# Optimization experiments

Hardware: AMD Instinct MI355X
Metric: run time of the kernel (lower is better)

The kernel has to match this reference:

```python
import jax, jax.numpy as jnp
from jax import lax
import numpy as np


def _fps(xyz, M):
    # Farthest point sampling: sequential over M steps, vectorized over batch.
    B, N, _ = xyz.shape
    def body(carry, _):
        dists, far = carry                       # dists:[B,N], far:[B]
        c = xyz[jnp.arange(B), far]              # [B,3] current centroid
        d = jnp.sum((xyz - c[:, None, :]) ** 2, axis=-1)
        dists = jnp.minimum(dists, d)
        nxt = jnp.argmax(dists, axis=-1).astype(jnp.int32)
        return (dists, nxt), far
    init = (jnp.full((B, N), 1e10, xyz.dtype), jnp.zeros((B,), jnp.int32))
    _, inds = lax.scan(body, init, None, length=M)
    return inds.T                                # [B, M]


def _ball_query(xyz, new_xyz, radius, K):
    # For each centroid pick first K point indices within radius; pad with first hit.
    N = xyz.shape[1]
    d2 = jnp.sum((new_xyz[:, :, None, :] - xyz[:, None, :, :]) ** 2, axis=-1)  # [B,M,N]
    ids = jnp.where(d2 <= radius * radius, jnp.arange(N)[None, None, :], N)
    ids = jnp.sort(ids, axis=-1)[..., :K]        # [B,M,K]
    return jnp.where(ids == N, ids[..., :1], ids)


_gather = jax.vmap(lambda p, i: p[i])            # p:[N,C], i:[M,K] -> [M,K,C]


def _mlp(x, layers):
    # Shared per-point MLP (1x1 conv + ReLU chain); BN omitted as in source head.
    for w, b in layers:
        x = jax.nn.relu(jnp.einsum('bmkc,cd->bmkd', x, w) + b)
    return x


def _sa(xyz, points, M, radius, K, layers):
    # Set-abstraction: FPS -> ball query -> group (centered xyz ++ feats) -> MLP -> max over K.
    fi = _fps(xyz, M)                                        # [B,M]
    new_xyz = jnp.take_along_axis(xyz, fi[..., None], axis=1)  # [B,M,3]
    gi = _ball_query(xyz, new_xyz, radius, K)                # [B,M,K]
    g_xyz = _gather(xyz, gi) - new_xyz[:, :, None, :]        # [B,M,K,3]
    g = jnp.concatenate([g_xyz, _gather(points, gi)], axis=-1)
    return new_xyz, jnp.max(_mlp(g, layers), axis=2)         # [B,M,Cout]


def _forward(xyz, points,
             w1a, b1a, w1b, b1b, w1c, b1c,
             w2a, b2a, w2b, b2b, w2c, b2c,
             w3a, b3a, w3b, b3b, w3c, b3c,
             lin1_w, lin2_w, cls_w, cls_b):
    B = xyz.shape[0]
    x1, f1 = _sa(xyz, points, 512, 0.2, 32, [(w1a, b1a), (w1b, b1b), (w1c, b1c)])
    x2, f2 = _sa(x1, f1, 128, 0.4, 64, [(w2a, b2a), (w2b, b2b), (w2c, b2c)])
    # group_all: single group containing all 128 points, feats = [xyz ++ points] (259 ch)
    g = jnp.concatenate([x2, f2], axis=-1)[:, None]           # [B,1,128,259]
    f3 = jnp.max(_mlp(g, [(w3a, b3a), (w3b, b3b), (w3c, b3c)]), axis=2)  # [B,1,1024]
    net = f3.reshape(B, -1)
    net = jax.nn.relu(net @ lin1_w)   # linear1 (no bias) + ReLU; dropout=identity (eval)
    net = jax.nn.relu(net @ lin2_w)
    return net @ cls_w + cls_b


def setup_inputs() -> dict:
    key = jax.random.key(0)
    ks = iter(jax.random.split(key, 40))
    B, N, NC = 32, 1024, 40
    inp = {}
    inp['xyz'] = jax.random.uniform(next(ks), (B, N, 3), jnp.float32, -1.0, 1.0)
    inp['points'] = jax.random.normal(next(ks), (B, N, 3), jnp.float32)
    def lin(cin, cout):
        w = jax.random.normal(next(ks), (cin, cout), jnp.float32) / np.float32(np.sqrt(cin))
        return w, jnp.zeros((cout,), jnp.float32)
    dims = {'1': [(6, 64), (64, 64), (64, 128)],
            '2': [(131, 128), (128, 128), (128, 256)],
            '3': [(259, 256), (256, 512), (512, 1024)]}
    for s, layer_dims in dims.items():
        for tag, (ci, co) in zip('abc', layer_dims):
            w, b = lin(ci, co)
            inp['w%s%s' % (s, tag)] = w
            inp['b%s%s' % (s, tag)] = b
    inp['lin1_w'] = jax.random.normal(next(ks), (1024, 512), jnp.float32) / np.float32(32.0)
    inp['lin2_w'] = jax.random.normal(next(ks), (512, 256), jnp.float32) / np.float32(np.sqrt(512))
    inp['cls_w'] = jax.random.normal(next(ks), (256, NC), jnp.float32) / np.float32(16.0)
    inp['cls_b'] = jnp.zeros((NC,), jnp.float32)
    return inp


def reference(xyz, points,
              w1a, b1a, w1b, b1b, w1c, b1c,
              w2a, b2a, w2b, b2b, w2c, b2c,
              w3a, b3a, w3b, b3b, w3c, b3c,
              lin1_w, lin2_w, cls_w, cls_b):
    return _forward(xyz, points,
                    w1a, b1a, w1b, b1b, w1c, b1c,
                    w2a, b2a, w2b, b2b, w2c, b2c,
                    w3a, b3a, w3b, b3b, w3c, b3c,
                    lin1_w, lin2_w, cls_w, cls_b)
```

## Files before the change

kernel.cpp:

```cpp
#include <hip/hip_runtime.h>

#define DEVFN __device__ __forceinline__

static inline int ceil_div(int a, int b) { return (a + b - 1) / b; }

typedef __attribute__((ext_vector_type(8))) short         bf16x8;
typedef __attribute__((ext_vector_type(4))) float         f32x4;
typedef __attribute__((ext_vector_type(8))) unsigned short u16x8;

DEVFN unsigned short f2bf(float x) {
    unsigned u = __float_as_uint(x);
    unsigned r = ((u >> 16) & 1u) + 0x7fffu;
    return (unsigned short)((u + r) >> 16);
}
DEVFN float bf2f(unsigned short h) { return __uint_as_float(((unsigned)h) << 16); }

template<int CTRL>
DEVFN double dpp_max_step(double v)
{
    int lo = __double2loint(v), hi = __double2hiint(v);
    int tlo = __builtin_amdgcn_update_dpp(lo, lo, CTRL, 0xF, 0xF, false);
    int thi = __builtin_amdgcn_update_dpp(hi, hi, CTRL, 0xF, 0xF, false);
    return fmax(v, __hiloint2double(thi, tlo));
}

template<int N>
__global__ __launch_bounds__(64) void fps_kernel(const float* __restrict__ xyz, int M,
                                                 int* __restrict__ out_idx,
                                                 float* __restrict__ nxout)
{
    constexpr int PPL = N / 64;
    int b = blockIdx.x, lane = threadIdx.x;
    __shared__ float4 sp[N];
    const float* p = xyz + (size_t)b * N * 3;
    float px[PPL], py[PPL], pz[PPL], dd[PPL];
    unsigned lo[PPL];
    #pragma unroll
    for (int j = 0; j < PPL; ++j) {
        int idx = lane + 64 * j;
        px[j] = p[idx*3+0]; py[j] = p[idx*3+1]; pz[j] = p[idx*3+2];
        sp[idx] = make_float4(px[j], py[j], pz[j], 0.f);
        dd[j] = 1e10f;
        lo[j] = ~(unsigned)idx;
    }
    __syncthreads();
    int far = 0;
    for (int s = 0; s < M; ++s) {
        float4 c4 = sp[far];
        if (lane == 0) {
            out_idx[(size_t)b*M + s] = far;
            nxout[((size_t)b*M + s)*3 + 0] = c4.x;
            nxout[((size_t)b*M + s)*3 + 1] = c4.y;
            nxout[((size_t)b*M + s)*3 + 2] = c4.z;
        }
        double cand[PPL];
        #pragma unroll
        for (int j = 0; j < PPL; ++j) {
            float dx = __fsub_rn(px[j], c4.x);
            float dy = __fsub_rn(py[j], c4.y);
            float dz = __fsub_rn(pz[j], c4.z);
            float d  = __fadd_rn(__fadd_rn(__fmul_rn(dx,dx), __fmul_rn(dy,dy)),
                                 __fmul_rn(dz,dz));
            float nd = fminf(dd[j], d);
            dd[j] = nd;
            cand[j] = __hiloint2double(__float_as_int(nd), (int)lo[j]);
        }
        #pragma unroll
        for (int st = PPL/2; st > 0; st >>= 1)
            #pragma unroll
            for (int j = 0; j < PPL; ++j)
                if (j < st) cand[j] = fmax(cand[j], cand[j + st]);
        double v = cand[0];
        v = dpp_max_step<0xB1>(v);
        v = dpp_max_step<0x4E>(v);
        v = dpp_max_step<0x124>(v);
        v = dpp_max_step<0x128>(v);
        v = dpp_max_step<0x142>(v);
        v = dpp_max_step<0x143>(v);
        int wlo = __builtin_amdgcn_readlane(__double2loint(v), 63);
        far = (int)(~(unsigned)wlo);
    }
}

__global__ void ballquery_kernel(const float* __restrict__ xyz,
                                 const float* __restrict__ new_xyz,
                                 int* __restrict__ gi,
                                 int B, int N, int M, int K, float r2)
{
    int t = blockIdx.x * blockDim.x + threadIdx.x;
    if (t >= B * M) return;
    int b = t / M;
    const float* p = xyz + (size_t)b * N * 3;
    float cx = new_xyz[t*3+0], cy = new_xyz[t*3+1], cz = new_xyz[t*3+2];
    int* out = gi + (size_t)t * K;
    int cnt = 0, first = 0;
    bool havefirst = false;
    for (int i = 0; i < N; ++i) {
        float dx = __fsub_rn(p[i*3+0], cx);
        float dy = __fsub_rn(p[i*3+1], cy);
        float dz = __fsub_rn(p[i*3+2], cz);
        float d  = __fadd_rn(__fadd_rn(__fmul_rn(dx,dx), __fmul_rn(dy,dy)),
                             __fmul_rn(dz,dz));
        if (d <= r2) {
            if (!havefirst) { first = i; havefirst = true; }
            out[cnt++] = i;
            if (cnt == K) break;
        }
    }
    for (; cnt < K; ++cnt) out[cnt] = first;
}

DEVFN float f4_elem(const float4& v, int u) {
    return u == 0 ? v.x : u == 1 ? v.y : u == 2 ? v.z : v.w;
}

__global__ void wsplit_kernel(const float* __restrict__ w,
                              unsigned short* __restrict__ wh,
                              unsigned short* __restrict__ wl, int CI, int CO)
{
    int t = blockIdx.x * 256 + threadIdx.x;
    if (t >= CI * CO) return;
    int co = t / CI, ci = t % CI;
    float v = w[(size_t)ci * CO + co];
    unsigned short h = f2bf(v);
    wh[t] = h;
    wl[t] = f2bf(v - bf2f(h));
}

__global__ void asplit_kernel(const float* __restrict__ a,
                              unsigned short* __restrict__ ah,
                              unsigned short* __restrict__ al, int n)
{
    int t = blockIdx.x * 256 + threadIdx.x;
    if (t >= n) return;
    float v = a[t];
    unsigned short h = f2bf(v);
    ah[t] = h;
    al[t] = f2bf(v - bf2f(h));
}

template<int CF, int CO, int KPTS>
__global__ __launch_bounds__(256) void sa_l1_kernel(
    const float* __restrict__ xyz, const float* __restrict__ feats,
    const float* __restrict__ new_xyz, const int* __restrict__ gi,
    const float* __restrict__ w, const float* __restrict__ bias,
    unsigned short* __restrict__ oh, unsigned short* __restrict__ ol,
    int N, int M, int row0)
{
    constexpr int WCH = CO / 4;
    const int lane = threadIdx.x & 63;
    const int wv   = __builtin_amdgcn_readfirstlane(threadIdx.x >> 6);
    const int rl   = blockIdx.x * 64 + lane;
    const int row  = row0 + rl;
    const int cent = row / KPTS;
    const int b    = cent / M;
    const int idx  = gi[row];
    const float* pp  = xyz + ((size_t)b*N + idx)*3;
    const float* cc3 = new_xyz + (size_t)cent*3;
    float a0 = __fsub_rn(pp[0], cc3[0]);
    float a1 = __fsub_rn(pp[1], cc3[1]);
    float a2 = __fsub_rn(pp[2], cc3[2]);
    const float* frow = feats + ((size_t)b*N + idx)*CF;
    const float* wcol = w + wv*WCH;
    const float* bcol = bias + wv*WCH;
    float acc[WCH];
    #pragma unroll
    for (int j = 0; j < WCH; ++j) acc[j] = bcol[j];
    #pragma unroll
    for (int j = 0; j < WCH; ++j) acc[j] += a0 * wcol[0*CO + j];
    #pragma unroll
    for (int j = 0; j < WCH; ++j) acc[j] += a1 * wcol[1*CO + j];
    #pragma unroll
    for (int j = 0; j < WCH; ++j) acc[j] += a2 * wcol[2*CO + j];
    constexpr int CF4 = CF & ~3;
    #pragma unroll 2
    for (int cc = 0; cc < CF4; cc += 4) {
        float4 a4 = *(const float4*)(frow + cc);
        #pragma unroll
        for (int u = 0; u < 4; ++u) {
            float a = f4_elem(a4, u);
            #pragma unroll
            for (int j = 0; j < WCH; ++j)
                acc[j] += a * wcol[(size_t)(3 + cc + u)*CO + j];
        }
    }
    #pragma unroll
    for (int f = CF4; f < CF; ++f) {
        float a = frow[f];
        #pragma unroll
        for (int j = 0; j < WCH; ++j)
            acc[j] += a * wcol[(size_t)(3 + f)*CO + j];
    }
    #pragma unroll
    for (int j8 = 0; j8 < WCH; j8 += 8) {
        u16x8 hv, lv;
        #pragma unroll
        for (int u = 0; u < 8; ++u) {
            float v = fmaxf(acc[j8+u], 0.f);
            unsigned short h = f2bf(v);
            hv[u] = (unsigned short)h;
            lv[u] = f2bf(v - bf2f(h));
        }
        size_t o = (size_t)rl*CO + wv*WCH + j8;
        *(u16x8*)(&oh[o]) = hv;
        *(u16x8*)(&ol[o]) = lv;
    }
}

template<int CI, int CO, int NTILE, int MROW, int KPTS, int OUTMODE>
__global__ __launch_bounds__(256) void mfma_layer_kernel(
    const unsigned short* __restrict__ ah, const unsigned short* __restrict__ al,
    const unsigned short* __restrict__ wh, const unsigned short* __restrict__ wl,
    const float* __restrict__ bias,
    unsigned short* __restrict__ oh, unsigned short* __restrict__ ol,
    float* __restrict__ ofp, int rowbase)
{
    constexpr int KT = CI / 32;
    static_assert(KT * MROW <= 16, "A-preload register budget");
    __shared__ float partial[4][OUTMODE == 2 ? MROW : 1][OUTMODE == 2 ? 16*NTILE : 1];
    const int wid  = threadIdx.x >> 6;
    const int lane = threadIdx.x & 63;
    const int m    = lane & 15;
    const int kg   = lane >> 4;
    const int blockrow = blockIdx.x * (64 * MROW);
    const int colbase  = blockIdx.y * (16 * NTILE);
    bf16x8 Ahf[MROW * KT], Alf[MROW * KT];
    #pragma unroll
    for (int t = 0; t < MROW; ++t) {
        const unsigned short* arh =
            ah + (size_t)(blockrow + t*64 + wid*16 + m) * CI + kg * 8;
        const unsigned short* arl =
            al + (size_t)(blockrow + t*64 + wid*16 + m) * CI + kg * 8;
        #pragma unroll
        for (int kt = 0; kt < KT; ++kt) {
            Ahf[t*KT + kt] = *(const bf16x8*)(arh + kt*32);
            Alf[t*KT + kt] = *(const bf16x8*)(arl + kt*32);
        }
    }
    #pragma unroll
    for (int nt = 0; nt < NTILE; ++nt) {
        f32x4 acc[MROW];
        #pragma unroll
        for (int t = 0; t < MROW; ++t) acc[t] = (f32x4){0.f, 0.f, 0.f, 0.f};
        const unsigned short* wbh = wh + (size_t)(colbase + nt*16 + m) * CI + kg * 8;
        const unsigned short* wbl = wl + (size_t)(colbase + nt*16 + m) * CI + kg * 8;
        #pragma unroll
        for (int kt = 0; kt < KT; ++kt) {
            bf16x8 Bh = *(const bf16x8*)(wbh + kt*32);
            bf16x8 Bl = *(const bf16x8*)(wbl + kt*32);
            #pragma unroll
            for (int t = 0; t < MROW; ++t) {
                acc[t] = __builtin_amdgcn_mfma_f32_16x16x32_bf16(Ahf[t*KT+kt], Bh, acc[t], 0, 0, 0);
                acc[t] = __builtin_amdgcn_mfma_f32_16x16x32_bf16(Ahf[t*KT+kt], Bl, acc[t], 0, 0, 0);
                acc[t] = __builtin_amdgcn_mfma_f32_16x16x32_bf16(Alf[t*KT+kt], Bh, acc[t], 0, 0, 0);
            }
        }
        int dcol = colbase + nt*16 + m;
        float bv = bias[dcol];
        #pragma unroll
        for (int t = 0; t < MROW; ++t) {
            float v[4];
            #pragma unroll
            for (int r = 0; r < 4; ++r) v[r] = fmaxf(acc[t][r] + bv, 0.f);
            if constexpr (OUTMODE == 0) {
                #pragma unroll
                for (int r = 0; r < 4; ++r) {
                    size_t o = (size_t)(blockrow + t*64 + wid*16 + kg*4 + r) * CO + dcol;
                    unsigned short h = f2bf(v[r]);
                    oh[o] = h;
                    ol[o] = f2bf(v[r] - bf2f(h));
                }
            } else if constexpr (OUTMODE == 1) {
                #pragma unroll
                for (int r = 0; r < 4; ++r)
                    ofp[(size_t)(blockrow + t*64 + wid*16 + kg*4 + r) * CO + dcol] = v[r];
            } else {
                float mx = fmaxf(fmaxf(v[0], v[1]), fmaxf(v[2], v[3]));
                mx = fmaxf(mx, __shfl_xor(mx, 16));
                mx = fmaxf(mx, __shfl_xor(mx, 32));
                if (lane < 16) partial[wid][t][nt*16 + m] = mx;
            }
        }
    }
    if constexpr (OUTMODE == 2) {
        __syncthreads();
        for (int c = threadIdx.x; c < 16*NTILE; c += 256) {
            #pragma unroll
            for (int t = 0; t < MROW; ++t) {
                if constexpr (KPTS == 64) {
                    float mx = fmaxf(fmaxf(partial[0][t][c], partial[1][t][c]),
                                     fmaxf(partial[2][t][c], partial[3][t][c]));
                    int cent = (rowbase + blockrow) / 64 + t;
                    ofp[(size_t)cent*CO + colbase + c] = mx;
                } else {
                    int cent0 = (rowbase + blockrow) / 32 + t*2;
                    ofp[(size_t)cent0*CO + colbase + c]     = fmaxf(partial[0][t][c], partial[1][t][c]);
                    ofp[(size_t)(cent0+1)*CO + colbase + c] = fmaxf(partial[2][t][c], partial[3][t][c]);
                }
            }
        }
    }
}

__global__ void concat_kernel(const float* __restrict__ a, const float* __restrict__ f,
                              float* __restrict__ out, int R, int CF)
{
    int C = CF + 3;
    int t = blockIdx.x * blockDim.x + threadIdx.x;
    if (t >= R * C) return;
    int r = t / C, c = t % C;
    out[t] = (c < 3) ? a[r*3 + c] : f[(size_t)r * CF + (c - 3)];
}

template<int RELU, int HASB>
__global__ __launch_bounds__(256) void gemm_kernel(
    const float* __restrict__ A, const float* __restrict__ W,
    const float* __restrict__ bias, float* __restrict__ Cc,
    int Mr, int Nc, int Kd)
{
    __shared__ float As[64][17];
    __shared__ float Ws[16][65];
    int tx = threadIdx.x % 16;
    int ty = threadIdx.x / 16;
    int row0 = blockIdx.y * 64;
    int col0 = blockIdx.x * 64;
    float acc[4][4] = {};
    for (int k0 = 0; k0 < Kd; k0 += 16) {
        for (int t = threadIdx.x; t < 64*16; t += 256) {
            int r = t >> 4, kk = t & 15;
            int gr = row0 + r, gk = k0 + kk;
            As[r][kk] = (gr < Mr && gk < Kd) ? A[(size_t)gr * Kd + gk] : 0.f;
        }
        for (int t = threadIdx.x; t < 16*64; t += 256) {
            int kk = t >> 6, c = t & 63;
            int gk = k0 + kk, gc = col0 + c;
            Ws[kk][c] = (gk < Kd && gc < Nc) ? W[(size_t)gk * Nc + gc] : 0.f;
        }
        __syncthreads();
        #pragma unroll
        for (int kk = 0; kk < 16; ++kk) {
            float av[4], wv[4];
            #pragma unroll
            for (int i = 0; i < 4; i++) av[i] = As[ty*4+i][kk];
            #pragma unroll
            for (int j = 0; j < 4; j++) wv[j] = Ws[kk][tx*4+j];
            #pragma unroll
            for (int i = 0; i < 4; i++)
                #pragma unroll
                for (int j = 0; j < 4; j++)
                    acc[i][j] += av[i] * wv[j];
        }
        __syncthreads();
    }
    #pragma unroll
    for (int i = 0; i < 4; i++) {
        int gr = row0 + ty*4 + i;
        if (gr >= Mr) continue;
        #pragma unroll
        for (int j = 0; j < 4; j++) {
            int gc = col0 + tx*4 + j;
            if (gc >= Nc) continue;
            float v = acc[i][j];
            if (HASB) v += bias[gc];
            if (RELU) v = fmaxf(v, 0.f);
            Cc[(size_t)gr * Nc + gc] = v;
        }
    }
}

template<int RELU, int HASB>
__global__ __launch_bounds__(256) void fc_kernel(
    const float* __restrict__ A, const float* __restrict__ W,
    const float* __restrict__ bias, float* __restrict__ Cc,
    int Mr, int Nc, int Kd)
{
    int t = blockIdx.x * 256 + threadIdx.x;
    if (t >= Mr * Nc) return;
    int row = t / Nc, col = t % Nc;
    const float* a = A + (size_t)row * Kd;
    const float* w = W + col;
    float acc = 0.f;
    #pragma unroll 8
    for (int k = 0; k < Kd; ++k)
        acc += a[k] * w[(size_t)k * Nc];
    if (HASB) acc += bias[col];
    if (RELU) acc = fmaxf(acc, 0.f);
    Cc[t] = acc;
}

__global__ void rowmax_kernel(const float* __restrict__ in, float* __restrict__ out,
                              int B, int P, int C)
{
    int t = blockIdx.x * blockDim.x + threadIdx.x;
    if (t >= B * C) return;
    int b = t / C, c = t % C;
    const float* p = in + (size_t)b * P * C + c;
    float mx = p[0];
    for (int i = 1; i < P; ++i) mx = fmaxf(mx, p[(size_t)i * C]);
    out[t] = mx;
}

extern "C" void kernel_launch(void* const* d_in, const int* in_sizes, int n_in,
                              void* d_out, int out_size, void* d_ws, size_t ws_size,
                              hipStream_t stream)
{
    const float* xyz    = (const float*)d_in[0];
    const float* points = (const float*)d_in[1];
    const float* w1a = (const float*)d_in[2];  const float* b1a = (const float*)d_in[3];
    const float* w1b = (const float*)d_in[4];  const float* b1b = (const float*)d_in[5];
    const float* w1c = (const float*)d_in[6];  const float* b1c = (const float*)d_in[7];
    const float* w2a = (const float*)d_in[8];  const float* b2a = (const float*)d_in[9];
    const float* w2b = (const float*)d_in[10]; const float* b2b = (const float*)d_in[11];
    const float* w2c = (const float*)d_in[12]; const float* b2c = (const float*)d_in[13];
    const float* w3a = (const float*)d_in[14]; const float* b3a = (const float*)d_in[15];
    const float* w3b = (const float*)d_in[16]; const float* b3b = (const float*)d_in[17];
    const float* w3c = (const float*)d_in[18]; const float* b3c = (const float*)d_in[19];
    const float* lin1 = (const float*)d_in[20];
    const float* lin2 = (const float*)d_in[21];
    const float* clsw = (const float*)d_in[22];
    const float* clsb = (const float*)d_in[23];

    char* ws = (char*)d_ws;
    size_t off = 0;
    auto alloc = [&](size_t bytes) -> void* {
        void* p = ws + off;
        off += (bytes + 255) & ~(size_t)255;
        return p;
    };
    int*   fps1 = (int*)  alloc((size_t)32*512*4);
    float* nx1  = (float*)alloc((size_t)32*512*3*4);
    int*   gi1  = (int*)  alloc((size_t)32*512*32*4);
    float* f1   = (float*)alloc((size_t)32*512*128*4);
    int*   fps2 = (int*)  alloc((size_t)32*128*4);
    float* nx2  = (float*)alloc((size_t)32*128*3*4);
    int*   gi2  = (int*)  alloc((size_t)32*128*64*4);
    float* f2   = (float*)alloc((size_t)32*128*256*4);
    float* g3   = (float*)alloc((size_t)4096*259*4);
    float* h3a  = (float*)alloc((size_t)4096*256*4);
    float* h3c  = (float*)alloc((size_t)4096*1024*4);
    float* f3   = (float*)alloc((size_t)32*1024*4);
    float* fc1  = (float*)alloc((size_t)32*512*4);
    float* fc2  = (float*)alloc((size_t)32*256*4);

    typedef unsigned short us;
    us* w1bh = (us*)alloc(64*64*2);     us* w1bl = (us*)alloc(64*64*2);
    us* w1ch = (us*)alloc(128*64*2);    us* w1cl = (us*)alloc(128*64*2);
    us* w2bh = (us*)alloc(128*128*2);   us* w2bl = (us*)alloc(128*128*2);
    us* w2ch = (us*)alloc(256*128*2);   us* w2cl = (us*)alloc(256*128*2);
    us* w3bh = (us*)alloc(512*256*2);   us* w3bl = (us*)alloc(512*256*2);
    us* w3ch = (us*)alloc(1024*512*2);  us* w3cl = (us*)alloc(1024*512*2);
    us* h3aH = (us*)alloc((size_t)4096*256*2);  us* h3aL = (us*)alloc((size_t)4096*256*2);
    us* h3bH = (us*)alloc((size_t)4096*512*2);  us* h3bL = (us*)alloc((size_t)4096*512*2);

    size_t avail = (ws_size > off + 1024) ? (ws_size - off - 1024) : 0;
    size_t bufcap = avail / 4;
    if (bufcap > (size_t)67200000) bufcap = 67200000;
    us* Ah = (us*)alloc(bufcap); us* Al = (us*)alloc(bufcap);
    us* Bh = (us*)alloc(bufcap); us* Bl = (us*)alloc(bufcap);

    auto wsp = [&](const float* w, int CI, int CO, us* wh, us* wl) {
        wsplit_kernel<<<ceil_div(CI*CO, 256), 256, 0, stream>>>(w, wh, wl, CI, CO);
    };
    wsp(w1b, 64, 64,  w1bh, w1bl);
    wsp(w1c, 64, 128, w1ch, w1cl);
    wsp(w2b, 128, 128, w2bh, w2bl);
    wsp(w2c, 128, 256, w2ch, w2cl);
    wsp(w3b, 256, 512, w3bh, w3bl);
    wsp(w3c, 512, 1024, w3ch, w3cl);

    fps_kernel<1024><<<32, 64, 0, stream>>>(xyz, 512, fps1, nx1);
    ballquery_kernel<<<ceil_div(32*512, 256), 256, 0, stream>>>(
        xyz, nx1, gi1, 32, 1024, 512, 32, (float)(0.2*0.2));
    {
        const int rows = 32*512*32;
        int ch = (int)((bufcap / (64*2)) & ~(size_t)255);
        if (ch > rows) ch = rows;
        if (ch < 256) ch = 256;
        for (int r0 = 0; r0 < rows; r0 += ch) {
            int rc = rows - r0 < ch ? rows - r0 : ch;
            sa_l1_kernel<3, 64, 32><<<rc/64, 256, 0, stream>>>(
                xyz, points, nx1, gi1, w1a, b1a, Ah, Al, 1024, 512, r0);
            mfma_layer_kernel<64, 64, 4, 4, 0, 0><<<dim3(rc/256, 1), 256, 0, stream>>>(
                Ah, Al, w1bh, w1bl, b1b, Bh, Bl, nullptr, 0);
            mfma_layer_kernel<64, 128, 8, 4, 32, 2><<<dim3(rc/256, 1), 256, 0, stream>>>(
                Bh, Bl, w1ch, w1cl, b1c, nullptr, nullptr, f1, r0);
        }
    }

    fps_kernel<512><<<32, 64, 0, stream>>>(nx1, 128, fps2, nx2);
    ballquery_kernel<<<ceil_div(32*128, 256), 256, 0, stream>>>(
        nx1, nx2, gi2, 32, 512, 128, 64, (float)(0.4*0.4));
    {
        const int rows = 32*128*64;
        int ch = (int)((bufcap / (128*2)) & ~(size_t)255);
        if (ch > rows) ch = rows;
        if (ch < 256) ch = 256;
        for (int r0 = 0; r0 < rows; r0 += ch) {
            int rc = rows - r0 < ch ? rows - r0 : ch;
            sa_l1_kernel<128, 128, 64><<<rc/64, 256, 0, stream>>>(
                nx1, f1, nx2, gi2, w2a, b2a, Ah, Al, 512, 128, r0);
            mfma_layer_kernel<128, 128, 8, 4, 0, 0><<<dim3(rc/256, 1), 256, 0, stream>>>(
                Ah, Al, w2bh, w2bl, b2b, Bh, Bl, nullptr, 0);
            mfma_layer_kernel<128, 256, 16, 4, 64, 2><<<dim3(rc/256, 1), 256, 0, stream>>>(
                Bh, Bl, w2ch, w2cl, b2c, nullptr, nullptr, f2, r0);
        }
    }

    concat_kernel<<<ceil_div(4096*259, 256), 256, 0, stream>>>(nx2, f2, g3, 4096, 256);
    {
        dim3 g(ceil_div(256, 64), ceil_div(4096, 64));
        gemm_kernel<1,1><<<g, 256, 0, stream>>>(g3, w3a, b3a, h3a, 4096, 256, 259);
    }
    asplit_kernel<<<ceil_div(4096*256, 256), 256, 0, stream>>>(h3a, h3aH, h3aL, 4096*256);
    mfma_layer_kernel<256, 512, 2, 2, 0, 0><<<dim3(4096/128, 512/32), 256, 0, stream>>>(
        h3aH, h3aL, w3bh, w3bl, b3b, h3bH, h3bL, nullptr, 0);
    mfma_layer_kernel<512, 1024, 4, 1, 0, 1><<<dim3(4096/64, 1024/64), 256, 0, stream>>>(
        h3bH, h3bL, w3ch, w3cl, b3c, nullptr, nullptr, h3c, 0);
    rowmax_kernel<<<ceil_div(32*1024, 256), 256, 0, stream>>>(h3c, f3, 32, 128, 1024);

    fc_kernel<1,0><<<ceil_div(32*512, 256), 256, 0, stream>>>(
        f3, lin1, nullptr, fc1, 32, 512, 1024);
    fc_kernel<1,0><<<ceil_div(32*256, 256), 256, 0, stream>>>(
        fc1, lin2, nullptr, fc2, 32, 256, 512);
    fc_kernel<0,1><<<ceil_div(32*40, 256), 256, 0, stream>>>(
        fc2, clsw, clsb, (float*)d_out, 32, 40, 256);
}
```

Baseline: 1.340 ms.

## Move SA2 first layer and SA3 first layer onto split-bf16 MFMA path

The SA2 first layer now runs on a new MFMA kernel that gathers pre-split bf16 hi/lo features of f1 and adds the xyz contribution with scalar FMAs. The SA1 last layer writes f1 directly as bf16 hi/lo. The SA3 first layer replaces the fp32 smem GEMM plus separate split kernel with a concat+split kernel padded to 288 channels and an MFMA layer. The aim is to move the remaining fp32 GEMMs onto matrix cores and drop intermediate fp32 buffers, at the cost of three-term bf16 split precision and padding work.

```diff
diff --git a/kernel.cpp b/kernel.cpp
--- a/kernel.cpp
+++ b/kernel.cpp
@@ -116,27 +116,17 @@
 
 __global__ void wsplit_kernel(const float* __restrict__ w,
                               unsigned short* __restrict__ wh,
-                              unsigned short* __restrict__ wl, int CI, int CO)
+                              unsigned short* __restrict__ wl,
+                              int CItot, int CO, int CIpad, int ro)
 {
     int t = blockIdx.x * 256 + threadIdx.x;
-    if (t >= CI * CO) return;
-    int co = t / CI, ci = t % CI;
-    float v = w[(size_t)ci * CO + co];
+    if (t >= CIpad * CO) return;
+    int co = t / CIpad, ci = t % CIpad;
+    int src = ci + ro;
+    float v = (src < CItot) ? w[(size_t)src * CO + co] : 0.f;
     unsigned short h = f2bf(v);
     wh[t] = h;
     wl[t] = f2bf(v - bf2f(h));
-}
-
-__global__ void asplit_kernel(const float* __restrict__ a,
-                              unsigned short* __restrict__ ah,
-                              unsigned short* __restrict__ al, int n)
-{
-    int t = blockIdx.x * 256 + threadIdx.x;
-    if (t >= n) return;
-    float v = a[t];
-    unsigned short h = f2bf(v);
-    ah[t] = h;
-    al[t] = f2bf(v - bf2f(h));
 }
 
 template<int CF, int CO, int KPTS>
@@ -216,8 +206,8 @@
     float* __restrict__ ofp, int rowbase)
 {
     constexpr int KT = CI / 32;
-    static_assert(KT * MROW <= 16, "A-preload register budget");
-    __shared__ float partial[4][OUTMODE == 2 ? MROW : 1][OUTMODE == 2 ? 16*NTILE : 1];
+    static_assert(KT * MROW <= 18, "A-preload register budget");
+    __shared__ float partial[4][OUTMODE >= 2 ? MROW : 1][OUTMODE >= 2 ? 16*NTILE : 1];
     const int wid  = threadIdx.x >> 6;
     const int lane = threadIdx.x & 63;
     const int m    = lane & 15;
@@ -282,7 +272,7 @@
             }
         }
     }
-    if constexpr (OUTMODE == 2) {
+    if constexpr (OUTMODE >= 2) {
         __syncthreads();
         for (int c = threadIdx.x; c < 16*NTILE; c += 256) {
             #pragma unroll
@@ -291,81 +281,132 @@
                     float mx = fmaxf(fmaxf(partial[0][t][c], partial[1][t][c]),
                                      fmaxf(partial[2][t][c], partial[3][t][c]));
                     int cent = (rowbase + blockrow) / 64 + t;
-                    ofp[(size_t)cent*CO + colbase + c] = mx;
+                    if constexpr (OUTMODE == 2) {
+                        ofp[(size_t)cent*CO + colbase + c] = mx;
+                    } else {
+                        size_t o = (size_t)cent*CO + colbase + c;
+                        unsigned short h = f2bf(mx);
+                        oh[o] = h; ol[o] = f2bf(mx - bf2f(h));
+                    }
                 } else {
                     int cent0 = (rowbase + blockrow) / 32 + t*2;
-                    ofp[(size_t)cent0*CO + colbase + c]     = fmaxf(partial[0][t][c], partial[1][t][c]);
-                    ofp[(size_t)(cent0+1)*CO + colbase + c] = fmaxf(partial[2][t][c], partial[3][t][c]);
+                    float v0 = fmaxf(partial[0][t][c], partial[1][t][c]);
+                    float v1 = fmaxf(partial[2][t][c], partial[3][t][c]);
+                    if constexpr (OUTMODE == 2) {
+                        ofp[(size_t)cent0*CO + colbase + c]     = v0;
+                        ofp[(size_t)(cent0+1)*CO + colbase + c] = v1;
+                    } else {
+                        size_t o0 = (size_t)cent0*CO + colbase + c;
+                        size_t o1 = (size_t)(cent0+1)*CO + colbase + c;
+                        unsigned short h0 = f2bf(v0), h1 = f2bf(v1);
+                        oh[o0] = h0; ol[o0] = f2bf(v0 - bf2f(h0));
+                        oh[o1] = h1; ol[o1] = f2bf(v1 - bf2f(h1));
+                    }
                 }
             }
         }
     }
 }
 
-__global__ void concat_kernel(const float* __restrict__ a, const float* __restrict__ f,
-                              float* __restrict__ out, int R, int CF)
-{
-    int C = CF + 3;
-    int t = blockIdx.x * blockDim.x + threadIdx.x;
-    if (t >= R * C) return;
-    int r = t / C, c = t % C;
-    out[t] = (c < 3) ? a[r*3 + c] : f[(size_t)r * CF + (c - 3)];
-}
-
-template<int RELU, int HASB>
-__global__ __launch_bounds__(256) void gemm_kernel(
-    const float* __restrict__ A, const float* __restrict__ W,
-    const float* __restrict__ bias, float* __restrict__ Cc,
-    int Mr, int Nc, int Kd)
-{
-    __shared__ float As[64][17];
-    __shared__ float Ws[16][65];
-    int tx = threadIdx.x % 16;
-    int ty = threadIdx.x / 16;
-    int row0 = blockIdx.y * 64;
-    int col0 = blockIdx.x * 64;
-    float acc[4][4] = {};
-    for (int k0 = 0; k0 < Kd; k0 += 16) {
-        for (int t = threadIdx.x; t < 64*16; t += 256) {
-            int r = t >> 4, kk = t & 15;
-            int gr = row0 + r, gk = k0 + kk;
-            As[r][kk] = (gr < Mr && gk < Kd) ? A[(size_t)gr * Kd + gk] : 0.f;
-        }
-        for (int t = threadIdx.x; t < 16*64; t += 256) {
-            int kk = t >> 6, c = t & 63;
-            int gk = k0 + kk, gc = col0 + c;
-            Ws[kk][c] = (gk < Kd && gc < Nc) ? W[(size_t)gk * Nc + gc] : 0.f;
-        }
-        __syncthreads();
-        #pragma unroll
-        for (int kk = 0; kk < 16; ++kk) {
-            float av[4], wv[4];
-            #pragma unroll
-            for (int i = 0; i < 4; i++) av[i] = As[ty*4+i][kk];
-            #pragma unroll
-            for (int j = 0; j < 4; j++) wv[j] = Ws[kk][tx*4+j];
-            #pragma unroll
-            for (int i = 0; i < 4; i++)
-                #pragma unroll
-                for (int j = 0; j < 4; j++)
-                    acc[i][j] += av[i] * wv[j];
-        }
-        __syncthreads();
-    }
-    #pragma unroll
-    for (int i = 0; i < 4; i++) {
-        int gr = row0 + ty*4 + i;
-        if (gr >= Mr) continue;
-        #pragma unroll
-        for (int j = 0; j < 4; j++) {
-            int gc = col0 + tx*4 + j;
-            if (gc >= Nc) continue;
-            float v = acc[i][j];
-            if (HASB) v += bias[gc];
-            if (RELU) v = fmaxf(v, 0.f);
-            Cc[(size_t)gr * Nc + gc] = v;
-        }
-    }
+template<int NTILE, int MROW>
+__global__ __launch_bounds__(256) void mfma_sa2l1_kernel(
+    const float* __restrict__ sxyz,
+    const float* __restrict__ cxyz,
+    const int* __restrict__ gi,
+    const unsigned short* __restrict__ f1h, const unsigned short* __restrict__ f1l,
+    const float* __restrict__ w,
+    const unsigned short* __restrict__ wh, const unsigned short* __restrict__ wl,
+    const float* __restrict__ bias,
+    unsigned short* __restrict__ oh, unsigned short* __restrict__ ol,
+    int rowbase)
+{
+    constexpr int CI = 128, CO = 128, KT = 4, KPTS = 64, M = 128, N = 512;
+    const int wid  = threadIdx.x >> 6;
+    const int lane = threadIdx.x & 63;
+    const int m    = lane & 15;
+    const int kg   = lane >> 4;
+    const int blockrow = blockIdx.x * (64 * MROW);
+    const int colbase  = blockIdx.y * (16 * NTILE);
+    bf16x8 Ahf[MROW * KT], Alf[MROW * KT];
+    #pragma unroll
+    for (int t = 0; t < MROW; ++t) {
+        int grow = rowbase + blockrow + t*64 + wid*16 + m;
+        int cent = grow / KPTS;
+        int b    = cent / M;
+        int idx  = gi[grow];
+        const unsigned short* arh = f1h + ((size_t)b*N + idx) * CI + kg * 8;
+        const unsigned short* arl = f1l + ((size_t)b*N + idx) * CI + kg * 8;
+        #pragma unroll
+        for (int kt = 0; kt < KT; ++kt) {
+            Ahf[t*KT + kt] = *(const bf16x8*)(arh + kt*32);
+            Alf[t*KT + kt] = *(const bf16x8*)(arl + kt*32);
+        }
+    }
+    float dx[MROW][4], dy[MROW][4], dz[MROW][4];
+    #pragma unroll
+    for (int t = 0; t < MROW; ++t)
+        #pragma unroll
+        for (int r = 0; r < 4; ++r) {
+            int grow = rowbase + blockrow + t*64 + wid*16 + kg*4 + r;
+            int cent = grow / KPTS;
+            int b    = cent / M;
+            int idx  = gi[grow];
+            const float* pp = sxyz + ((size_t)b*N + idx)*3;
+            const float* cc = cxyz + (size_t)cent*3;
+            dx[t][r] = __fsub_rn(pp[0], cc[0]);
+            dy[t][r] = __fsub_rn(pp[1], cc[1]);
+            dz[t][r] = __fsub_rn(pp[2], cc[2]);
+        }
+    #pragma unroll
+    for (int nt = 0; nt < NTILE; ++nt) {
+        f32x4 acc[MROW];
+        #pragma unroll
+        for (int t = 0; t < MROW; ++t) acc[t] = (f32x4){0.f, 0.f, 0.f, 0.f};
+        const unsigned short* wbh = wh + (size_t)(colbase + nt*16 + m) * CI + kg * 8;
+        const unsigned short* wbl = wl + (size_t)(colbase + nt*16 + m) * CI + kg * 8;
+        #pragma unroll
+        for (int kt = 0; kt < KT; ++kt) {
+            bf16x8 Bh = *(const bf16x8*)(wbh + kt*32);
+            bf16x8 Bl = *(const bf16x8*)(wbl + kt*32);
+            #pragma unroll
+            for (int t = 0; t < MROW; ++t) {
+                acc[t] = __builtin_amdgcn_mfma_f32_16x16x32_bf16(Ahf[t*KT+kt], Bh, acc[t], 0, 0, 0);
+                acc[t] = __builtin_amdgcn_mfma_f32_16x16x32_bf16(Ahf[t*KT+kt], Bl, acc[t], 0, 0, 0);
+                acc[t] = __builtin_amdgcn_mfma_f32_16x16x32_bf16(Alf[t*KT+kt], Bh, acc[t], 0, 0, 0);
+            }
+        }
+        int dcol = colbase + nt*16 + m;
+        float w0 = w[0*CO + dcol], w1 = w[1*CO + dcol], w2 = w[2*CO + dcol];
+        float bv = bias[dcol];
+        #pragma unroll
+        for (int t = 0; t < MROW; ++t)
+            #pragma unroll
+            for (int r = 0; r < 4; ++r) {
+                float v = acc[t][r] + bv + dx[t][r]*w0 + dy[t][r]*w1 + dz[t][r]*w2;
+                v = fmaxf(v, 0.f);
+                size_t o = (size_t)(blockrow + t*64 + wid*16 + kg*4 + r) * CO + dcol;
+                unsigned short h = f2bf(v);
+                oh[o] = h;
+                ol[o] = f2bf(v - bf2f(h));
+            }
+    }
+}
+
+__global__ void concat_split_kernel(const float* __restrict__ a, const float* __restrict__ f,
+                                    unsigned short* __restrict__ oh,
+                                    unsigned short* __restrict__ ol,
+                                    int R, int CF, int CIpad)
+{
+    int t = blockIdx.x * 256 + threadIdx.x;
+    if (t >= R * CIpad) return;
+    int r = t / CIpad, c = t % CIpad;
+    float v;
+    if (c < 3) v = a[r*3 + c];
+    else if (c < CF + 3) v = f[(size_t)r * CF + (c - 3)];
+    else v = 0.f;
+    unsigned short h = f2bf(v);
+    oh[t] = h;
+    ol[t] = f2bf(v - bf2f(h));
 }
 
 template<int RELU, int HASB>
@@ -430,13 +471,10 @@
     int*   fps1 = (int*)  alloc((size_t)32*512*4);
     float* nx1  = (float*)alloc((size_t)32*512*3*4);
     int*   gi1  = (int*)  alloc((size_t)32*512*32*4);
-    float* f1   = (float*)alloc((size_t)32*512*128*4);
     int*   fps2 = (int*)  alloc((size_t)32*128*4);
     float* nx2  = (float*)alloc((size_t)32*128*3*4);
     int*   gi2  = (int*)  alloc((size_t)32*128*64*4);
     float* f2   = (float*)alloc((size_t)32*128*256*4);
-    float* g3   = (float*)alloc((size_t)4096*259*4);
-    float* h3a  = (float*)alloc((size_t)4096*256*4);
     float* h3c  = (float*)alloc((size_t)4096*1024*4);
     float* f3   = (float*)alloc((size_t)32*1024*4);
     float* fc1  = (float*)alloc((size_t)32*512*4);
@@ -445,10 +483,15 @@
     typedef unsigned short us;
     us* w1bh = (us*)alloc(64*64*2);     us* w1bl = (us*)alloc(64*64*2);
     us* w1ch = (us*)alloc(128*64*2);    us* w1cl = (us*)alloc(128*64*2);
+    us* w2ah = (us*)alloc(128*128*2);   us* w2al = (us*)alloc(128*128*2);
     us* w2bh = (us*)alloc(128*128*2);   us* w2bl = (us*)alloc(128*128*2);
     us* w2ch = (us*)alloc(256*128*2);   us* w2cl = (us*)alloc(256*128*2);
+    us* w3ah = (us*)alloc(256*288*2);   us* w3al = (us*)alloc(256*288*2);
     us* w3bh = (us*)alloc(512*256*2);   us* w3bl = (us*)alloc(512*256*2);
     us* w3ch = (us*)alloc(1024*512*2);  us* w3cl = (us*)alloc(1024*512*2);
+    us* f1h  = (us*)alloc((size_t)16384*128*2);
+    us* f1l  = (us*)alloc((size_t)16384*128*2);
+    us* g3H  = (us*)alloc((size_t)4096*288*2);  us* g3L  = (us*)alloc((size_t)4096*288*2);
     us* h3aH = (us*)alloc((size_t)4096*256*2);  us* h3aL = (us*)alloc((size_t)4096*256*2);
     us* h3bH = (us*)alloc((size_t)4096*512*2);  us* h3bL = (us*)alloc((size_t)4096*512*2);
 
@@ -458,32 +501,34 @@
     us* Ah = (us*)alloc(bufcap); us* Al = (us*)alloc(bufcap);
     us* Bh = (us*)alloc(bufcap); us* Bl = (us*)alloc(bufcap);
 
-    auto wsp = [&](const float* w, int CI, int CO, us* wh, us* wl) {
-        wsplit_kernel<<<ceil_div(CI*CO, 256), 256, 0, stream>>>(w, wh, wl, CI, CO);
+    auto wsp = [&](const float* w, int CItot, int CO, int CIpad, int ro, us* wh, us* wl) {
+        wsplit_kernel<<<ceil_div(CIpad*CO, 256), 256, 0, stream>>>(w, wh, wl, CItot, CO, CIpad, ro);
     };
-    wsp(w1b, 64, 64,  w1bh, w1bl);
-    wsp(w1c, 64, 128, w1ch, w1cl);
-    wsp(w2b, 128, 128, w2bh, w2bl);
-    wsp(w2c, 128, 256, w2ch, w2cl);
-    wsp(w3b, 256, 512, w3bh, w3bl);
-    wsp(w3c, 512, 1024, w3ch, w3cl);
+    wsp(w1b, 64, 64, 64, 0,   w1bh, w1bl);
+    wsp(w1c, 64, 128, 64, 0,  w1ch, w1cl);
+    wsp(w2a, 131, 128, 128, 3, w2ah, w2al);
+    wsp(w2b, 128, 128, 128, 0, w2bh, w2bl);
+    wsp(w2c, 128, 256, 128, 0, w2ch, w2cl);
+    wsp(w3a, 259, 256, 288, 0, w3ah, w3al);
+    wsp(w3b, 256, 512, 256, 0, w3bh, w3bl);
+    wsp(w3c, 512, 1024, 512, 0, w3ch, w3cl);
 
     fps_kernel<1024><<<32, 64, 0, stream>>>(xyz, 512, fps1, nx1);
     ballquery_kernel<<<ceil_div(32*512, 256), 256, 0, stream>>>(
         xyz, nx1, gi1, 32, 1024, 512, 32, (float)(0.2*0.2));
     {
         const int rows = 32*512*32;
-        int ch = (int)((bufcap / (64*2)) & ~(size_t)255);
+        int ch = (int)((bufcap / (64*2)) & ~(size_t)1023);
         if (ch > rows) ch = rows;
-        if (ch < 256) ch = 256;
+        if (ch < 1024) ch = 1024;
         for (int r0 = 0; r0 < rows; r0 += ch) {
             int rc = rows - r0 < ch ? rows - r0 : ch;
             sa_l1_kernel<3, 64, 32><<<rc/64, 256, 0, stream>>>(
                 xyz, points, nx1, gi1, w1a, b1a, Ah, Al, 1024, 512, r0);
             mfma_layer_kernel<64, 64, 4, 4, 0, 0><<<dim3(rc/256, 1), 256, 0, stream>>>(
                 Ah, Al, w1bh, w1bl, b1b, Bh, Bl, nullptr, 0);
-            mfma_layer_kernel<64, 128, 8, 4, 32, 2><<<dim3(rc/256, 1), 256, 0, stream>>>(
-                Bh, Bl, w1ch, w1cl, b1c, nullptr, nullptr, f1, r0);
+            mfma_layer_kernel<64, 128, 8, 4, 32, 3><<<dim3(rc/256, 1), 256, 0, stream>>>(
+                Bh, Bl, w1ch, w1cl, b1c, f1h, f1l, nullptr, r0);
         }
     }
 
@@ -492,13 +537,13 @@
         nx1, nx2, gi2, 32, 512, 128, 64, (float)(0.4*0.4));
     {
         const int rows = 32*128*64;
-        int ch = (int)((bufcap / (128*2)) & ~(size_t)255);
+        int ch = (int)((bufcap / (128*2)) & ~(size_t)1023);
         if (ch > rows) ch = rows;
-        if (ch < 256) ch = 256;
+        if (ch < 1024) ch = 1024;
         for (int r0 = 0; r0 < rows; r0 += ch) {
             int rc = rows - r0 < ch ? rows - r0 : ch;
-            sa_l1_kernel<128, 128, 64><<<rc/64, 256, 0, stream>>>(
-                nx1, f1, nx2, gi2, w2a, b2a, Ah, Al, 512, 128, r0);
+            mfma_sa2l1_kernel<8, 2><<<dim3(rc/128, 1), 256, 0, stream>>>(
+                nx1, nx2, gi2, f1h, f1l, w2a, w2ah, w2al, b2a, Ah, Al, r0);
             mfma_layer_kernel<128, 128, 8, 4, 0, 0><<<dim3(rc/256, 1), 256, 0, stream>>>(
                 Ah, Al, w2bh, w2bl, b2b, Bh, Bl, nullptr, 0);
             mfma_layer_kernel<128, 256, 16, 4, 64, 2><<<dim3(rc/256, 1), 256, 0, stream>>>(
@@ -506,12 +551,10 @@
         }
     }
 
-    concat_kernel<<<ceil_div(4096*259, 256), 256, 0, stream>>>(nx2, f2, g3, 4096, 256);
-    {
-        dim3 g(ceil_div(256, 64), ceil_div(4096, 64));
-        gemm_kernel<1,1><<<g, 256, 0, stream>>>(g3, w3a, b3a, h3a, 4096, 256, 259);
-    }
-    asplit_kernel<<<ceil_div(4096*256, 256), 256, 0, stream>>>(h3a, h3aH, h3aL, 4096*256);
+    concat_split_kernel<<<ceil_div(4096*288, 256), 256, 0, stream>>>(
+        nx2, f2, g3H, g3L, 4096, 256, 288);
+    mfma_layer_kernel<288, 256, 2, 1, 0, 0><<<dim3(4096/64, 256/32), 256, 0, stream>>>(
+        g3H, g3L, w3ah, w3al, b3a, h3aH, h3aL, nullptr, 0);
     mfma_layer_kernel<256, 512, 2, 2, 0, 0><<<dim3(4096/128, 512/32), 256, 0, stream>>>(
         h3aH, h3aL, w3bh, w3bl, b3b, h3bH, h3bL, nullptr, 0);
     mfma_layer_kernel<512, 1024, 4, 1, 0, 1><<<dim3(4096/64, 1024/64), 256, 0, stream>>>(
```

Result: faster. 1.262 ms (-5.8%).
